# Kernel tuning notes

Measured on AMD Instinct MI355X. Metric: run time of the kernel, lower is better.

Reference implementation:

```python
import jax, jax.numpy as jnp
import numpy as np

B, N, I, D, K = 64, 16, 2048, 32, 32  # batch, num_capsule, input_num_capsule, dim_capsule, input_dim_capsule
ROUTINGS = 3
EPS = 1e-07


def squash(s):
    # squared_norm includes per-element eps before the sum, matching torch code
    sq = jnp.sum(s * s + EPS, axis=-1, keepdims=True)
    return sq * s / ((1.0 + sq) * jnp.sqrt(sq))


def setup_inputs() -> dict:
    key = jax.random.key(0)
    kx, kw = jax.random.split(key)
    x = jax.random.normal(kx, (B, I, K), dtype=jnp.float32)
    # xavier_uniform over a [N, I, D, K] tensor: fan_in = D*K (last two dims treated as matrix by torch init? torch treats dim1.. as fan) -- use gain=1 uniform bound per torch's convention: fan_in = I*D*K/... Use simple xavier over (fan_in=K, fan_out=D) receptive field I*N.
    fan_in = I * K
    fan_out = I * D  # torch: fan_in = size(1)*receptive, here just use uniform bound from full-tensor xavier
    bound = float(np.sqrt(6.0 / (fan_in + fan_out)))
    W = jax.random.uniform(kw, (N, I, D, K), minval=-bound, maxval=bound, dtype=jnp.float32)
    return {"x": x, "W": W}


def reference(x, W):
    # u_hat[b,n,i,d] = sum_k W[n,i,d,k] * x[b,i,k]
    u_hat = jnp.einsum('nidk,bik->bnid', W, x)
    b = jnp.zeros((B, N, I), dtype=u_hat.dtype)
    v = None
    for r in range(ROUTINGS):
        c = jax.nn.softmax(b, axis=1)                 # softmax over num_capsule
        s = jnp.einsum('bni,bnid->bnd', c, u_hat)     # [B, N, D]
        v = squash(s)
        if r < ROUTINGS - 1:
            a = jnp.einsum('bnid,bnd->bni', u_hat, v)
            b = b + a
    return v  # [B, N, D]
```

## Files before the change

kernel.cpp:

```cpp
#include <hip/hip_runtime.h>
#include <stdint.h>

#define Bdim 64
#define Ndim 16
#define Idim 2048
#define Ddim 32
#define Kdim 32
#define EPSV 1e-7f

#define TILE_I   4
#define TILES_PB 16
#define NB_Y     (Idim / (TILE_I * TILES_PB))

typedef __attribute__((ext_vector_type(8))) short short8v;
typedef __attribute__((ext_vector_type(4))) float f32x4;

static __device__ __forceinline__ unsigned pk_rne(float a, float b) {
    unsigned ua = __float_as_uint(a);
    unsigned ub = __float_as_uint(b);
    ua = (ua + 0x7fffu + ((ua >> 16) & 1u)) >> 16;
    ub = (ub + 0x7fffu + ((ub >> 16) & 1u)) >> 16;
    return (ua & 0xffffu) | (ub << 16);
}
static __device__ __forceinline__ float bf2f(unsigned us) {
    return __uint_as_float(us << 16);
}

#define GLL16(g, s)                                                              \
    __builtin_amdgcn_global_load_lds(                                            \
        (const __attribute__((address_space(1))) void*)(uintptr_t)(const void*)(g), \
        (__attribute__((address_space(3))) void*)(uintptr_t)(void*)(s), 16, 0, 0)

__global__ __launch_bounds__(256) void convert_x(
    const float* __restrict__ x, unsigned short* __restrict__ x2)
{
    const int i  = blockIdx.x;
    const int b  = threadIdx.x >> 2;
    const int ko = threadIdx.x & 3;
    const float* src = x + ((size_t)b * Idim + i) * Kdim + (ko << 3);
    float4 a = ((const float4*)src)[0];
    float4 c = ((const float4*)src)[1];
    uint4 o;
    o.x = pk_rne(a.x, a.y); o.y = pk_rne(a.z, a.w);
    o.z = pk_rne(c.x, c.y); o.w = pk_rne(c.z, c.w);
    *(uint4*)(x2 + ((size_t)i * 64 + b) * 32 + (ko << 3)) = o;
}

__global__ __launch_bounds__(256) void pass1_dma(
    const float* __restrict__ W, const unsigned short* __restrict__ x2,
    unsigned short* __restrict__ uhat, float* __restrict__ s0)
{
    __shared__ float          ldsW[2][TILE_I * 1024];
    __shared__ unsigned short ldsX[2][TILE_I * 2048];

    const int n     = blockIdx.x;
    const int iblk0 = blockIdx.y * (TILE_I * TILES_PB);
    const int tid   = threadIdx.x;
    const int l     = tid & 63;
    const int bcol  = ((tid >> 6) << 4) + (l & 15);
    const int krow  = l >> 4;

    const float*          Wblk = W  + ((size_t)n * Idim + iblk0) * (Ddim * Kdim);
    const unsigned short* Xblk = x2 + (size_t)iblk0 * (64 * 32);

    f32x4 acc0 = {0.f, 0.f, 0.f, 0.f};
    f32x4 acc1 = {0.f, 0.f, 0.f, 0.f};
    const f32x4 zero = {0.f, 0.f, 0.f, 0.f};

    auto stage = [&](int t, int buf) {
        const float* Wt = Wblk + (size_t)t * (TILE_I * 1024);
        float* dw = &ldsW[buf][0];
        #pragma unroll
        for (int j = 0; j < 4; ++j) {
            const int c  = j * 256 + tid;
            const int lc = c & 63, h = (c >> 6) & 1, mt = (c >> 7) & 1, il = c >> 8;
            const float* src = Wt + il * 1024 + ((mt << 4) + (lc & 15)) * 32
                                  + ((lc >> 4) << 3) + (h << 2);
            GLL16(src, dw + (size_t)c * 4);
        }
        const unsigned short* Xt = Xblk + (size_t)t * (TILE_I * 2048);
        unsigned short* dx = &ldsX[buf][0];
        #pragma unroll
        for (int j = 0; j < 4; ++j) {
            const int c = j * 256 + tid;
            GLL16(Xt + (size_t)c * 8, dx + (size_t)c * 8);
        }
    };

    stage(0, 0);

    for (int t = 0; t < TILES_PB; ++t) {
        if (t + 1 < TILES_PB) stage(t + 1, (t + 1) & 1);
        asm volatile("s_waitcnt vmcnt(8)" ::: "memory");
        __builtin_amdgcn_s_barrier();
        __builtin_amdgcn_sched_barrier(0);

        const float*          lw = &ldsW[t & 1][0];
        const unsigned short* lx = &ldsX[t & 1][0];
        const int ibase = iblk0 + t * TILE_I;

        #pragma unroll
        for (int il = 0; il < TILE_I; ++il) {
            const int i = ibase + il;

            union { short8v v; unsigned u[4]; } bf, af0, af1;
            bf.v = *(const short8v*)(lx + il * 2048 + bcol * 32 + (krow << 3));

            const float4 w00 = *(const float4*)(lw + ((il * 256 + l)       << 2));
            const float4 w01 = *(const float4*)(lw + ((il * 256 + 64 + l)  << 2));
            const float4 w10 = *(const float4*)(lw + ((il * 256 + 128 + l) << 2));
            const float4 w11 = *(const float4*)(lw + ((il * 256 + 192 + l) << 2));
            af0.u[0] = pk_rne(w00.x, w00.y); af0.u[1] = pk_rne(w00.z, w00.w);
            af0.u[2] = pk_rne(w01.x, w01.y); af0.u[3] = pk_rne(w01.z, w01.w);
            af1.u[0] = pk_rne(w10.x, w10.y); af1.u[1] = pk_rne(w10.z, w10.w);
            af1.u[2] = pk_rne(w11.x, w11.y); af1.u[3] = pk_rne(w11.z, w11.w);

            f32x4 c0 = __builtin_amdgcn_mfma_f32_16x16x32_bf16(af0.v, bf.v, zero, 0, 0, 0);
            f32x4 c1 = __builtin_amdgcn_mfma_f32_16x16x32_bf16(af1.v, bf.v, zero, 0, 0, 0);

            const size_t ubase = (((size_t)i * Ndim + n) * 64 + bcol) * Ddim + (krow << 2);
            uint2 p0; p0.x = pk_rne(c0[0], c0[1]); p0.y = pk_rne(c0[2], c0[3]);
            *(uint2*)(uhat + ubase) = p0;
            uint2 p1; p1.x = pk_rne(c1[0], c1[1]); p1.y = pk_rne(c1[2], c1[3]);
            *(uint2*)(uhat + ubase + 16) = p1;

            acc0 += c0;
            acc1 += c1;
        }
        asm volatile("s_waitcnt lgkmcnt(0)" ::: "memory");
        __builtin_amdgcn_s_barrier();
        __builtin_amdgcn_sched_barrier(0);
    }

    float* sp = s0 + ((size_t)bcol * Ndim + n) * Ddim + (krow << 2);
    #pragma unroll
    for (int r = 0; r < 4; ++r) atomicAdd(sp + r, acc0[r]);
    #pragma unroll
    for (int r = 0; r < 4; ++r) atomicAdd(sp + 16 + r, acc1[r]);
}

__global__ __launch_bounds__(256) void pass1_simple(
    const float* __restrict__ W, const float* __restrict__ x,
    unsigned short* __restrict__ uhat, float* __restrict__ s0, int bbase, int Bc)
{
    const int IB = 16;
    const int n  = blockIdx.x;
    const int i0 = blockIdx.y * IB;
    const int w  = threadIdx.x >> 6;
    const int l  = threadIdx.x & 63;
    const int bcol  = (w << 4) + (l & 15);
    const int bglob = bbase + bcol;
    const int krow  = l >> 4;

    f32x4 acc0 = {0.f,0.f,0.f,0.f}, acc1 = {0.f,0.f,0.f,0.f};
    const f32x4 zero = {0.f,0.f,0.f,0.f};

    for (int ii = 0; ii < IB; ++ii) {
        const int i = i0 + ii;
        const float* xp = x + ((size_t)bglob * Idim + i) * Kdim + (krow << 3);
        float4 xa = ((const float4*)xp)[0];
        float4 xb = ((const float4*)xp)[1];
        union { short8v v; unsigned u[4]; } bf, af0, af1;
        bf.u[0]=pk_rne(xa.x,xa.y); bf.u[1]=pk_rne(xa.z,xa.w);
        bf.u[2]=pk_rne(xb.x,xb.y); bf.u[3]=pk_rne(xb.z,xb.w);

        const float* wbase = W + ((size_t)n * Idim + i) * Ddim * Kdim + (krow << 3);
        const float* wp0 = wbase + (size_t)(l & 15) * Kdim;
        float4 wa = ((const float4*)wp0)[0];
        float4 wb = ((const float4*)wp0)[1];
        af0.u[0]=pk_rne(wa.x,wa.y); af0.u[1]=pk_rne(wa.z,wa.w);
        af0.u[2]=pk_rne(wb.x,wb.y); af0.u[3]=pk_rne(wb.z,wb.w);
        const float* wp1 = wp0 + 16 * Kdim;
        float4 wc = ((const float4*)wp1)[0];
        float4 wd = ((const float4*)wp1)[1];
        af1.u[0]=pk_rne(wc.x,wc.y); af1.u[1]=pk_rne(wc.z,wc.w);
        af1.u[2]=pk_rne(wd.x,wd.y); af1.u[3]=pk_rne(wd.z,wd.w);

        f32x4 c0 = __builtin_amdgcn_mfma_f32_16x16x32_bf16(af0.v, bf.v, zero, 0,0,0);
        f32x4 c1 = __builtin_amdgcn_mfma_f32_16x16x32_bf16(af1.v, bf.v, zero, 0,0,0);

        const size_t ubase = (((size_t)i * Ndim + n) * Bc + bcol) * Ddim + (krow << 2);
        uint2 p0; p0.x=pk_rne(c0[0],c0[1]); p0.y=pk_rne(c0[2],c0[3]);
        *(uint2*)(uhat + ubase) = p0;
        uint2 p1; p1.x=pk_rne(c1[0],c1[1]); p1.y=pk_rne(c1[2],c1[3]);
        *(uint2*)(uhat + ubase + 16) = p1;
        acc0 += c0; acc1 += c1;
    }
    float* sp = s0 + ((size_t)bglob * Ndim + n) * Ddim + (krow << 2);
    #pragma unroll
    for (int r = 0; r < 4; ++r) atomicAdd(sp + r, acc0[r]);
    #pragma unroll
    for (int r = 0; r < 4; ++r) atomicAdd(sp + 16 + r, acc1[r]);
}

template<int FIRST>
__global__ __launch_bounds__(256) void route_kernel(
    const unsigned short* __restrict__ uhat, const float* __restrict__ vin,
    float* __restrict__ bbuf, float* __restrict__ sout, int bbase, int Bc)
{
    const int bc = blockIdx.x;
    const int it = blockIdx.y;
    const int w = threadIdx.x >> 6;
    const int l = threadIdx.x & 63;
    const int g = l >> 2, q = l & 3;
    const int bglob = bbase + bc;

    const float* vp = vin + ((size_t)bglob * Ndim + g) * Ddim + (q << 3);
    float vreg[8];
    *(float4*)&vreg[0] = ((const float4*)vp)[0];
    *(float4*)&vreg[4] = ((const float4*)vp)[1];

    float sacc[8];
    #pragma unroll
    for (int j = 0; j < 8; ++j) sacc[j] = 0.f;

    for (int ii = w; ii < 128; ii += 4) {
        const int i = (it << 7) + ii;
        const unsigned short* up = uhat + (((size_t)i * Ndim + g) * Bc + bc) * Ddim + (q << 3);
        uint4 uraw = *(const uint4*)up;
        float u[8];
        u[0] = bf2f(uraw.x & 0xffffu); u[1] = bf2f(uraw.x >> 16);
        u[2] = bf2f(uraw.y & 0xffffu); u[3] = bf2f(uraw.y >> 16);
        u[4] = bf2f(uraw.z & 0xffffu); u[5] = bf2f(uraw.z >> 16);
        u[6] = bf2f(uraw.w & 0xffffu); u[7] = bf2f(uraw.w >> 16);

        float p = 0.f;
        #pragma unroll
        for (int j = 0; j < 8; ++j) p = fmaf(u[j], vreg[j], p);
        p += __shfl_xor(p, 1);
        p += __shfl_xor(p, 2);

        float logit = p;
        if (FIRST) {
            if (q == 0) bbuf[((size_t)bc * Idim + i) * Ndim + g] = p;
        } else {
            logit += bbuf[((size_t)bc * Idim + i) * Ndim + g];
        }
        float m = logit;
        m = fmaxf(m, __shfl_xor(m, 4));
        m = fmaxf(m, __shfl_xor(m, 8));
        m = fmaxf(m, __shfl_xor(m, 16));
        m = fmaxf(m, __shfl_xor(m, 32));
        float e = __expf(logit - m);
        float z = e;
        z += __shfl_xor(z, 4);
        z += __shfl_xor(z, 8);
        z += __shfl_xor(z, 16);
        z += __shfl_xor(z, 32);
        float c = e / z;

        #pragma unroll
        for (int j = 0; j < 8; ++j) sacc[j] = fmaf(c, u[j], sacc[j]);
    }

    __shared__ float sl[4][512];
    #pragma unroll
    for (int j = 0; j < 8; ++j) sl[w][(l << 3) + j] = sacc[j];
    __syncthreads();
    for (int e2 = threadIdx.x; e2 < 512; e2 += 256) {
        float vsum = sl[0][e2] + sl[1][e2] + sl[2][e2] + sl[3][e2];
        atomicAdd(sout + (size_t)bglob * (Ndim * Ddim) + e2, vsum);
    }
}

__global__ __launch_bounds__(256) void squash_kernel(
    const float* __restrict__ s, float* __restrict__ vout, float scale, int bbase)
{
    const int tid = blockIdx.x * 256 + threadIdx.x;
    const int row = tid >> 5;
    const int d   = tid & 31;
    const size_t off = ((size_t)bbase * Ndim + row) * Ddim + d;
    float sv = s[off] * scale;
    float t = fmaf(sv, sv, EPSV);
    t += __shfl_xor(t, 1);
    t += __shfl_xor(t, 2);
    t += __shfl_xor(t, 4);
    t += __shfl_xor(t, 8);
    t += __shfl_xor(t, 16);
    float vv = sv * t / ((1.f + t) * sqrtf(t));
    vout[off] = vv;
}

extern "C" void kernel_launch(void* const* d_in, const int* in_sizes, int n_in,
                              void* d_out, int out_size, void* d_ws, size_t ws_size,
                              hipStream_t stream)
{
    (void)in_sizes; (void)n_in; (void)out_size;
    const float* x = (const float*)d_in[0];
    const float* W = (const float*)d_in[1];
    float* out = (float*)d_out;

    const size_t snd = (size_t)Bdim * Ndim * Ddim;
    const size_t fixed = 5 * snd * sizeof(float);

    int Bc = 64;
    while (Bc > 16) {
        size_t need = (size_t)Bc * Idim * Ndim * Ddim * 2 + (size_t)Bc * Idim * Ndim * 4 + fixed;
        if (need <= ws_size) break;
        Bc >>= 1;
    }

    char* p = (char*)d_ws;
    unsigned short* uhat = (unsigned short*)p; p += (size_t)Bc * Idim * Ndim * Ddim * 2;
    float* bbuf = (float*)p;                   p += (size_t)Bc * Idim * Ndim * 4;
    float* sbuf = (float*)p;
    float* s0 = sbuf;
    float* s1 = sbuf + snd;
    float* s2 = sbuf + 2 * snd;
    float* v0 = sbuf + 3 * snd;
    float* v1 = sbuf + 4 * snd;

    for (int bbase = 0; bbase < Bdim; bbase += Bc) {
        (void)hipMemsetAsync(sbuf, 0, 3 * snd * sizeof(float), stream);

        if (Bc == 64) {
            unsigned short* x2 = (unsigned short*)bbuf;
            convert_x<<<dim3(Idim), 256, 0, stream>>>(x, x2);
            pass1_dma<<<dim3(Ndim, NB_Y), 256, 0, stream>>>(W, x2, uhat, s0);
        } else {
            pass1_simple<<<dim3(Ndim, Idim / 16), dim3(64 * (Bc / 16)), 0, stream>>>(
                W, x, uhat, s0, bbase, Bc);
        }
        squash_kernel<<<dim3(Bc * 2), 256, 0, stream>>>(s0, v0, 1.f / 16.f, bbase);

        route_kernel<1><<<dim3(Bc, Idim / 128), 256, 0, stream>>>(uhat, v0, bbuf, s1, bbase, Bc);
        squash_kernel<<<dim3(Bc * 2), 256, 0, stream>>>(s1, v1, 1.f, bbase);

        route_kernel<0><<<dim3(Bc, Idim / 128), 256, 0, stream>>>(uhat, v1, bbuf, s2, bbase, Bc);
        squash_kernel<<<dim3(Bc * 2), 256, 0, stream>>>(s2, out, 1.f, bbase);
    }
}
```

Measured before the change: 169.9 us.

## Deepen prefetch in GEMM tile loop and batch loads in routing loop

In the u_hat GEMM kernel, the wait on outstanding global-to-LDS loads is relaxed in middle iterations so the next tile's transfers stay in flight while the current tile is consumed. In the routing kernel, the per-i loop is restructured to issue four u_hat vector loads and four logit loads up front before computing, which raises memory-level parallelism and hides latency. This costs extra registers and, if the vmcnt accounting is wrong, could read LDS data before it has arrived.

```diff
diff --git a/kernel.cpp b/kernel.cpp
--- a/kernel.cpp
+++ b/kernel.cpp
@@ -91,7 +91,11 @@
 
     for (int t = 0; t < TILES_PB; ++t) {
         if (t + 1 < TILES_PB) stage(t + 1, (t + 1) & 1);
-        asm volatile("s_waitcnt vmcnt(8)" ::: "memory");
+        if (t == 0 || t == TILES_PB - 1) {
+            asm volatile("s_waitcnt vmcnt(8)" ::: "memory");
+        } else {
+            asm volatile("s_waitcnt vmcnt(16)" ::: "memory");
+        }
         __builtin_amdgcn_s_barrier();
         __builtin_amdgcn_sched_barrier(0);
 
@@ -214,43 +218,55 @@
     #pragma unroll
     for (int j = 0; j < 8; ++j) sacc[j] = 0.f;
 
-    for (int ii = w; ii < 128; ii += 4) {
-        const int i = (it << 7) + ii;
-        const unsigned short* up = uhat + (((size_t)i * Ndim + g) * Bc + bc) * Ddim + (q << 3);
-        uint4 uraw = *(const uint4*)up;
-        float u[8];
-        u[0] = bf2f(uraw.x & 0xffffu); u[1] = bf2f(uraw.x >> 16);
-        u[2] = bf2f(uraw.y & 0xffffu); u[3] = bf2f(uraw.y >> 16);
-        u[4] = bf2f(uraw.z & 0xffffu); u[5] = bf2f(uraw.z >> 16);
-        u[6] = bf2f(uraw.w & 0xffffu); u[7] = bf2f(uraw.w >> 16);
-
-        float p = 0.f;
-        #pragma unroll
-        for (int j = 0; j < 8; ++j) p = fmaf(u[j], vreg[j], p);
-        p += __shfl_xor(p, 1);
-        p += __shfl_xor(p, 2);
-
-        float logit = p;
-        if (FIRST) {
-            if (q == 0) bbuf[((size_t)bc * Idim + i) * Ndim + g] = p;
-        } else {
-            logit += bbuf[((size_t)bc * Idim + i) * Ndim + g];
-        }
-        float m = logit;
-        m = fmaxf(m, __shfl_xor(m, 4));
-        m = fmaxf(m, __shfl_xor(m, 8));
-        m = fmaxf(m, __shfl_xor(m, 16));
-        m = fmaxf(m, __shfl_xor(m, 32));
-        float e = __expf(logit - m);
-        float z = e;
-        z += __shfl_xor(z, 4);
-        z += __shfl_xor(z, 8);
-        z += __shfl_xor(z, 16);
-        z += __shfl_xor(z, 32);
-        float c = e / z;
-
-        #pragma unroll
-        for (int j = 0; j < 8; ++j) sacc[j] = fmaf(c, u[j], sacc[j]);
+    for (int base = 0; base < 128; base += 16) {
+        const int i0v = (it << 7) + base + w;
+
+        uint4 ur[4];
+        float bl[4];
+        #pragma unroll
+        for (int j = 0; j < 4; ++j) {
+            const int i = i0v + 4 * j;
+            ur[j] = *(const uint4*)(uhat + (((size_t)i * Ndim + g) * Bc + bc) * Ddim + (q << 3));
+            if (!FIRST) bl[j] = bbuf[((size_t)bc * Idim + i) * Ndim + g];
+        }
+
+        #pragma unroll
+        for (int j = 0; j < 4; ++j) {
+            const int i = i0v + 4 * j;
+            float u[8];
+            u[0] = bf2f(ur[j].x & 0xffffu); u[1] = bf2f(ur[j].x >> 16);
+            u[2] = bf2f(ur[j].y & 0xffffu); u[3] = bf2f(ur[j].y >> 16);
+            u[4] = bf2f(ur[j].z & 0xffffu); u[5] = bf2f(ur[j].z >> 16);
+            u[6] = bf2f(ur[j].w & 0xffffu); u[7] = bf2f(ur[j].w >> 16);
+
+            float p = 0.f;
+            #pragma unroll
+            for (int k = 0; k < 8; ++k) p = fmaf(u[k], vreg[k], p);
+            p += __shfl_xor(p, 1);
+            p += __shfl_xor(p, 2);
+
+            float logit = p;
+            if (FIRST) {
+                if (q == 0) bbuf[((size_t)bc * Idim + i) * Ndim + g] = p;
+            } else {
+                logit += bl[j];
+            }
+            float m = logit;
+            m = fmaxf(m, __shfl_xor(m, 4));
+            m = fmaxf(m, __shfl_xor(m, 8));
+            m = fmaxf(m, __shfl_xor(m, 16));
+            m = fmaxf(m, __shfl_xor(m, 32));
+            float e = __expf(logit - m);
+            float z = e;
+            z += __shfl_xor(z, 4);
+            z += __shfl_xor(z, 8);
+            z += __shfl_xor(z, 16);
+            z += __shfl_xor(z, 32);
+            float c = e / z;
+
+            #pragma unroll
+            for (int k = 0; k < 8; ++k) sacc[k] = fmaf(c, u[k], sacc[k]);
+        }
     }
 
     __shared__ float sl[4][512];
```

Result: slower. 175.6 us (+3.3%).

## Restructure pass1 to keep x tile resident and loop over capsules per block

Applied to the files above, without the earlier changes.

pass1_dma now assigns each 512-thread block a fixed block of 8 input capsules and loops over all 16 output capsules. The bf16 x tile is loaded into LDS once and reused across every n, while W tiles for successive n are double-buffered. Each wave computes one of the two 16-row D halves instead of both. The intent is to stop reloading x for every capsule and to raise per-block parallelism. In exchange the kernel launches fewer blocks, uses more LDS per block, and issues atomic adds into s0 once per capsule per block.

```diff
diff --git a/kernel.cpp b/kernel.cpp
--- a/kernel.cpp
+++ b/kernel.cpp
@@ -8,9 +8,7 @@
 #define Kdim 32
 #define EPSV 1e-7f
 
-#define TILE_I   4
-#define TILES_PB 16
-#define NB_Y     (Idim / (TILE_I * TILES_PB))
+#define IBLK8 8
 
 typedef __attribute__((ext_vector_type(8))) short short8v;
 typedef __attribute__((ext_vector_type(4))) float f32x4;
@@ -46,97 +44,93 @@
     *(uint4*)(x2 + ((size_t)i * 64 + b) * 32 + (ko << 3)) = o;
 }
 
-__global__ __launch_bounds__(256) void pass1_dma(
+__global__ __launch_bounds__(512) void pass1_dma(
     const float* __restrict__ W, const unsigned short* __restrict__ x2,
     unsigned short* __restrict__ uhat, float* __restrict__ s0)
 {
-    __shared__ float          ldsW[2][TILE_I * 1024];
-    __shared__ unsigned short ldsX[2][TILE_I * 2048];
-
-    const int n     = blockIdx.x;
-    const int iblk0 = blockIdx.y * (TILE_I * TILES_PB);
-    const int tid   = threadIdx.x;
-    const int l     = tid & 63;
-    const int bcol  = ((tid >> 6) << 4) + (l & 15);
-    const int krow  = l >> 4;
-
-    const float*          Wblk = W  + ((size_t)n * Idim + iblk0) * (Ddim * Kdim);
-    const unsigned short* Xblk = x2 + (size_t)iblk0 * (64 * 32);
-
-    f32x4 acc0 = {0.f, 0.f, 0.f, 0.f};
-    f32x4 acc1 = {0.f, 0.f, 0.f, 0.f};
+    __shared__ float          ldsW[2][IBLK8 * 1024];
+    __shared__ unsigned short ldsX[IBLK8 * 2048];
+
+    const int i0   = blockIdx.x * IBLK8;
+    const int tid  = threadIdx.x;
+    const int w    = tid >> 6;
+    const int l    = tid & 63;
+    const int brg  = w >> 1;
+    const int mt   = w & 1;
+    const int bcol = (brg << 4) + (l & 15);
+    const int krow = l >> 4;
+
     const f32x4 zero = {0.f, 0.f, 0.f, 0.f};
 
-    auto stage = [&](int t, int buf) {
-        const float* Wt = Wblk + (size_t)t * (TILE_I * 1024);
+    auto stageW = [&](int n, int buf) {
+        const float* Wt = W + ((size_t)n * Idim + i0) * 1024;
         float* dw = &ldsW[buf][0];
         #pragma unroll
         for (int j = 0; j < 4; ++j) {
-            const int c  = j * 256 + tid;
-            const int lc = c & 63, h = (c >> 6) & 1, mt = (c >> 7) & 1, il = c >> 8;
-            const float* src = Wt + il * 1024 + ((mt << 4) + (lc & 15)) * 32
-                                  + ((lc >> 4) << 3) + (h << 2);
-            GLL16(src, dw + (size_t)c * 4);
-        }
-        const unsigned short* Xt = Xblk + (size_t)t * (TILE_I * 2048);
-        unsigned short* dx = &ldsX[buf][0];
+            const int g   = w * 4 + j;
+            const int il  = g >> 2, mtc = (g >> 1) & 1, h = g & 1;
+            const float* src = Wt + il * 1024 + ((mtc << 4) + (l & 15)) * 32
+                                  + ((l >> 4) << 3) + (h << 2);
+            GLL16(src, dw + ((size_t)(g * 64 + l)) * 4);
+        }
+    };
+
+    {
+        const unsigned short* Xt = x2 + (size_t)i0 * 2048;
         #pragma unroll
         for (int j = 0; j < 4; ++j) {
-            const int c = j * 256 + tid;
-            GLL16(Xt + (size_t)c * 8, dx + (size_t)c * 8);
-        }
-    };
-
-    stage(0, 0);
-
-    for (int t = 0; t < TILES_PB; ++t) {
-        if (t + 1 < TILES_PB) stage(t + 1, (t + 1) & 1);
-        asm volatile("s_waitcnt vmcnt(8)" ::: "memory");
+            const int c = (w * 4 + j) * 64 + l;
+            GLL16(Xt + (size_t)c * 8, &ldsX[0] + (size_t)c * 8);
+        }
+        stageW(0, 0);
+        asm volatile("s_waitcnt vmcnt(0)" ::: "memory");
         __builtin_amdgcn_s_barrier();
         __builtin_amdgcn_sched_barrier(0);
-
-        const float*          lw = &ldsW[t & 1][0];
-        const unsigned short* lx = &ldsX[t & 1][0];
-        const int ibase = iblk0 + t * TILE_I;
-
-        #pragma unroll
-        for (int il = 0; il < TILE_I; ++il) {
-            const int i = ibase + il;
-
-            union { short8v v; unsigned u[4]; } bf, af0, af1;
-            bf.v = *(const short8v*)(lx + il * 2048 + bcol * 32 + (krow << 3));
-
-            const float4 w00 = *(const float4*)(lw + ((il * 256 + l)       << 2));
-            const float4 w01 = *(const float4*)(lw + ((il * 256 + 64 + l)  << 2));
-            const float4 w10 = *(const float4*)(lw + ((il * 256 + 128 + l) << 2));
-            const float4 w11 = *(const float4*)(lw + ((il * 256 + 192 + l) << 2));
-            af0.u[0] = pk_rne(w00.x, w00.y); af0.u[1] = pk_rne(w00.z, w00.w);
-            af0.u[2] = pk_rne(w01.x, w01.y); af0.u[3] = pk_rne(w01.z, w01.w);
-            af1.u[0] = pk_rne(w10.x, w10.y); af1.u[1] = pk_rne(w10.z, w10.w);
-            af1.u[2] = pk_rne(w11.x, w11.y); af1.u[3] = pk_rne(w11.z, w11.w);
-
-            f32x4 c0 = __builtin_amdgcn_mfma_f32_16x16x32_bf16(af0.v, bf.v, zero, 0, 0, 0);
-            f32x4 c1 = __builtin_amdgcn_mfma_f32_16x16x32_bf16(af1.v, bf.v, zero, 0, 0, 0);
-
-            const size_t ubase = (((size_t)i * Ndim + n) * 64 + bcol) * Ddim + (krow << 2);
-            uint2 p0; p0.x = pk_rne(c0[0], c0[1]); p0.y = pk_rne(c0[2], c0[3]);
-            *(uint2*)(uhat + ubase) = p0;
-            uint2 p1; p1.x = pk_rne(c1[0], c1[1]); p1.y = pk_rne(c1[2], c1[3]);
-            *(uint2*)(uhat + ubase + 16) = p1;
-
-            acc0 += c0;
-            acc1 += c1;
-        }
+    }
+
+    for (int n = 0; n < Ndim; ++n) {
+        if (n + 1 < Ndim) stageW(n + 1, (n + 1) & 1);
+        if (n == Ndim - 1) {
+            asm volatile("s_waitcnt vmcnt(12)" ::: "memory");
+        } else {
+            asm volatile("s_waitcnt vmcnt(16)" ::: "memory");
+        }
+        __builtin_amdgcn_s_barrier();
+        __builtin_amdgcn_sched_barrier(0);
+
+        const float* lw = &ldsW[n & 1][0];
+        f32x4 acc = {0.f, 0.f, 0.f, 0.f};
+
+        #pragma unroll
+        for (int il = 0; il < IBLK8; ++il) {
+            const int i = i0 + il;
+
+            union { short8v v; unsigned u[4]; } bf, af;
+            bf.v = *(const short8v*)(&ldsX[0] + il * 2048 + bcol * 32 + (krow << 3));
+
+            const float4 wa = *(const float4*)(lw + ((size_t)(((il << 2) + (mt << 1) + 0) * 64 + l)) * 4);
+            const float4 wb = *(const float4*)(lw + ((size_t)(((il << 2) + (mt << 1) + 1) * 64 + l)) * 4);
+            af.u[0] = pk_rne(wa.x, wa.y); af.u[1] = pk_rne(wa.z, wa.w);
+            af.u[2] = pk_rne(wb.x, wb.y); af.u[3] = pk_rne(wb.z, wb.w);
+
+            f32x4 c = __builtin_amdgcn_mfma_f32_16x16x32_bf16(af.v, bf.v, zero, 0, 0, 0);
+
+            const size_t ubase = (((size_t)i * Ndim + n) * 64 + bcol) * Ddim
+                                 + (mt << 4) + (krow << 2);
+            uint2 p; p.x = pk_rne(c[0], c[1]); p.y = pk_rne(c[2], c[3]);
+            *(uint2*)(uhat + ubase) = p;
+
+            acc += c;
+        }
+
+        float* sp = s0 + ((size_t)bcol * Ndim + n) * Ddim + (mt << 4) + (krow << 2);
+        #pragma unroll
+        for (int r = 0; r < 4; ++r) atomicAdd(sp + r, acc[r]);
+
         asm volatile("s_waitcnt lgkmcnt(0)" ::: "memory");
         __builtin_amdgcn_s_barrier();
         __builtin_amdgcn_sched_barrier(0);
     }
-
-    float* sp = s0 + ((size_t)bcol * Ndim + n) * Ddim + (krow << 2);
-    #pragma unroll
-    for (int r = 0; r < 4; ++r) atomicAdd(sp + r, acc0[r]);
-    #pragma unroll
-    for (int r = 0; r < 4; ++r) atomicAdd(sp + 16 + r, acc1[r]);
 }
 
 __global__ __launch_bounds__(256) void pass1_simple(
@@ -316,7 +310,7 @@
         if (Bc == 64) {
             unsigned short* x2 = (unsigned short*)bbuf;
             convert_x<<<dim3(Idim), 256, 0, stream>>>(x, x2);
-            pass1_dma<<<dim3(Ndim, NB_Y), 256, 0, stream>>>(W, x2, uhat, s0);
+            pass1_dma<<<dim3(Idim / IBLK8), 512, 0, stream>>>(W, x2, uhat, s0);
         } else {
             pass1_simple<<<dim3(Ndim, Idim / 16), dim3(64 * (Bc / 16)), 0, stream>>>(
                 W, x, uhat, s0, bbase, Bc);
```

New measurement: 327.3 us. 1.93x slower.

## Restructure pass1 blocks to cover four capsules and reuse staged x tiles

Applied to the files above, without the earlier changes.

The u_hat pass is retiled so that each 512-thread block handles 4 output capsules over 32 input capsules. It used to handle one capsule over 64. The bf16 x tile for each group of 4 input capsules is now staged once and reused across the 4 capsules, while W slices stream through a double buffer. Each pair of waves splits the input capsules, and their partial s0 sums are combined through LDS before the atomics, which halves the atomic traffic per block. The grid shrinks from 16x32 to 4x64 blocks. This adds more barriers per unit of work and a fine-grained vmcnt schedule that must stay correct.

```diff
diff --git a/kernel.cpp b/kernel.cpp
--- a/kernel.cpp
+++ b/kernel.cpp
@@ -7,10 +7,6 @@
 #define Ddim 32
 #define Kdim 32
 #define EPSV 1e-7f
-
-#define TILE_I   4
-#define TILES_PB 16
-#define NB_Y     (Idim / (TILE_I * TILES_PB))
 
 typedef __attribute__((ext_vector_type(8))) short short8v;
 typedef __attribute__((ext_vector_type(4))) float f32x4;
@@ -46,97 +42,133 @@
     *(uint4*)(x2 + ((size_t)i * 64 + b) * 32 + (ko << 3)) = o;
 }
 
-__global__ __launch_bounds__(256) void pass1_dma(
+__global__ __launch_bounds__(512) void pass1_dma(
     const float* __restrict__ W, const unsigned short* __restrict__ x2,
     unsigned short* __restrict__ uhat, float* __restrict__ s0)
 {
-    __shared__ float          ldsW[2][TILE_I * 1024];
-    __shared__ unsigned short ldsX[2][TILE_I * 2048];
-
-    const int n     = blockIdx.x;
-    const int iblk0 = blockIdx.y * (TILE_I * TILES_PB);
+    __shared__ float          ldsW[2][4 * 1024];
+    __shared__ unsigned short ldsX[2][4 * 2048];
+
+    const int nbase = blockIdx.x * 4;
+    const int i0    = blockIdx.y * 32;
     const int tid   = threadIdx.x;
+    const int w     = tid >> 6;
     const int l     = tid & 63;
-    const int bcol  = ((tid >> 6) << 4) + (l & 15);
+    const int brg   = w >> 1;
+    const int ih    = w & 1;
+    const int bcol  = (brg << 4) + (l & 15);
     const int krow  = l >> 4;
 
-    const float*          Wblk = W  + ((size_t)n * Idim + iblk0) * (Ddim * Kdim);
-    const unsigned short* Xblk = x2 + (size_t)iblk0 * (64 * 32);
-
-    f32x4 acc0 = {0.f, 0.f, 0.f, 0.f};
-    f32x4 acc1 = {0.f, 0.f, 0.f, 0.f};
     const f32x4 zero = {0.f, 0.f, 0.f, 0.f};
-
-    auto stage = [&](int t, int buf) {
-        const float* Wt = Wblk + (size_t)t * (TILE_I * 1024);
-        float* dw = &ldsW[buf][0];
-        #pragma unroll
-        for (int j = 0; j < 4; ++j) {
-            const int c  = j * 256 + tid;
-            const int lc = c & 63, h = (c >> 6) & 1, mt = (c >> 7) & 1, il = c >> 8;
-            const float* src = Wt + il * 1024 + ((mt << 4) + (lc & 15)) * 32
+    f32x4 acc[4][2];
+    #pragma unroll
+    for (int n = 0; n < 4; ++n) { acc[n][0] = zero; acc[n][1] = zero; }
+
+    auto stageW = [&](int uu) {
+        const int sn = uu & 3, ss = uu >> 2;
+        const float* Wq = W + (((size_t)(nbase + sn) * Idim) + i0 + ss * 4) * 1024;
+        float* dw = &ldsW[uu & 1][0];
+        #pragma unroll
+        for (int j = 0; j < 2; ++j) {
+            const int c  = j * 512 + tid;
+            const int lc = c & 63, h = (c >> 6) & 1, mtc = (c >> 7) & 1, il = c >> 8;
+            const float* src = Wq + il * 1024 + ((mtc << 4) + (lc & 15)) * 32
                                   + ((lc >> 4) << 3) + (h << 2);
             GLL16(src, dw + (size_t)c * 4);
         }
-        const unsigned short* Xt = Xblk + (size_t)t * (TILE_I * 2048);
-        unsigned short* dx = &ldsX[buf][0];
-        #pragma unroll
-        for (int j = 0; j < 4; ++j) {
-            const int c = j * 256 + tid;
-            GLL16(Xt + (size_t)c * 8, dx + (size_t)c * 8);
-        }
     };
-
-    stage(0, 0);
-
-    for (int t = 0; t < TILES_PB; ++t) {
-        if (t + 1 < TILES_PB) stage(t + 1, (t + 1) & 1);
-        asm volatile("s_waitcnt vmcnt(8)" ::: "memory");
-        __builtin_amdgcn_s_barrier();
-        __builtin_amdgcn_sched_barrier(0);
-
-        const float*          lw = &ldsW[t & 1][0];
-        const unsigned short* lx = &ldsX[t & 1][0];
-        const int ibase = iblk0 + t * TILE_I;
-
-        #pragma unroll
-        for (int il = 0; il < TILE_I; ++il) {
-            const int i = ibase + il;
-
-            union { short8v v; unsigned u[4]; } bf, af0, af1;
-            bf.v = *(const short8v*)(lx + il * 2048 + bcol * 32 + (krow << 3));
-
-            const float4 w00 = *(const float4*)(lw + ((il * 256 + l)       << 2));
-            const float4 w01 = *(const float4*)(lw + ((il * 256 + 64 + l)  << 2));
-            const float4 w10 = *(const float4*)(lw + ((il * 256 + 128 + l) << 2));
-            const float4 w11 = *(const float4*)(lw + ((il * 256 + 192 + l) << 2));
-            af0.u[0] = pk_rne(w00.x, w00.y); af0.u[1] = pk_rne(w00.z, w00.w);
-            af0.u[2] = pk_rne(w01.x, w01.y); af0.u[3] = pk_rne(w01.z, w01.w);
-            af1.u[0] = pk_rne(w10.x, w10.y); af1.u[1] = pk_rne(w10.z, w10.w);
-            af1.u[2] = pk_rne(w11.x, w11.y); af1.u[3] = pk_rne(w11.z, w11.w);
-
-            f32x4 c0 = __builtin_amdgcn_mfma_f32_16x16x32_bf16(af0.v, bf.v, zero, 0, 0, 0);
-            f32x4 c1 = __builtin_amdgcn_mfma_f32_16x16x32_bf16(af1.v, bf.v, zero, 0, 0, 0);
-
-            const size_t ubase = (((size_t)i * Ndim + n) * 64 + bcol) * Ddim + (krow << 2);
-            uint2 p0; p0.x = pk_rne(c0[0], c0[1]); p0.y = pk_rne(c0[2], c0[3]);
-            *(uint2*)(uhat + ubase) = p0;
-            uint2 p1; p1.x = pk_rne(c1[0], c1[1]); p1.y = pk_rne(c1[2], c1[3]);
-            *(uint2*)(uhat + ubase + 16) = p1;
-
-            acc0 += c0;
-            acc1 += c1;
-        }
-        asm volatile("s_waitcnt lgkmcnt(0)" ::: "memory");
-        __builtin_amdgcn_s_barrier();
-        __builtin_amdgcn_sched_barrier(0);
-    }
-
-    float* sp = s0 + ((size_t)bcol * Ndim + n) * Ddim + (krow << 2);
-    #pragma unroll
-    for (int r = 0; r < 4; ++r) atomicAdd(sp + r, acc0[r]);
-    #pragma unroll
-    for (int r = 0; r < 4; ++r) atomicAdd(sp + 16 + r, acc1[r]);
+    auto stageX = [&](int ss) {
+        const unsigned short* Xq = x2 + ((size_t)(i0 + ss * 4)) * 2048;
+        unsigned short* dx = &ldsX[ss & 1][0];
+        #pragma unroll
+        for (int j = 0; j < 2; ++j) {
+            const int c = j * 512 + tid;
+            GLL16(Xq + (size_t)c * 8, dx + (size_t)c * 8);
+        }
+    };
+
+    stageX(0); stageW(0);
+    asm volatile("s_waitcnt vmcnt(0)" ::: "memory");
+    __builtin_amdgcn_s_barrier();
+    __builtin_amdgcn_sched_barrier(0);
+
+    for (int s = 0; s < 8; ++s) {
+        #pragma unroll
+        for (int n = 0; n < 4; ++n) {
+            const int u = s * 4 + n;
+            const bool last = (u == 31);
+            if (!last) {
+                stageW(u + 1);
+                if (n == 3) stageX(s + 1);
+            }
+            if (last)        { asm volatile("s_waitcnt vmcnt(4)" ::: "memory"); }
+            else if (n == 3) { asm volatile("s_waitcnt vmcnt(8)" ::: "memory"); }
+            else             { asm volatile("s_waitcnt vmcnt(6)" ::: "memory"); }
+            __builtin_amdgcn_s_barrier();
+            __builtin_amdgcn_sched_barrier(0);
+
+            const float*          lw = &ldsW[u & 1][0];
+            const unsigned short* lx = &ldsX[s & 1][0];
+            const int ng = nbase + n;
+
+            #pragma unroll
+            for (int il2 = 0; il2 < 2; ++il2) {
+                const int il = (ih << 1) + il2;
+                const int i  = i0 + s * 4 + il;
+
+                union { short8v v; unsigned u4[4]; } bf, af0, af1;
+                bf.v = *(const short8v*)(lx + il * 2048 + bcol * 32 + (krow << 3));
+
+                const float4 w00 = *(const float4*)(lw + ((il * 256 + l)       << 2));
+                const float4 w01 = *(const float4*)(lw + ((il * 256 + 64 + l)  << 2));
+                const float4 w10 = *(const float4*)(lw + ((il * 256 + 128 + l) << 2));
+                const float4 w11 = *(const float4*)(lw + ((il * 256 + 192 + l) << 2));
+                af0.u4[0] = pk_rne(w00.x, w00.y); af0.u4[1] = pk_rne(w00.z, w00.w);
+                af0.u4[2] = pk_rne(w01.x, w01.y); af0.u4[3] = pk_rne(w01.z, w01.w);
+                af1.u4[0] = pk_rne(w10.x, w10.y); af1.u4[1] = pk_rne(w10.z, w10.w);
+                af1.u4[2] = pk_rne(w11.x, w11.y); af1.u4[3] = pk_rne(w11.z, w11.w);
+
+                f32x4 c0 = __builtin_amdgcn_mfma_f32_16x16x32_bf16(af0.v, bf.v, zero, 0, 0, 0);
+                f32x4 c1 = __builtin_amdgcn_mfma_f32_16x16x32_bf16(af1.v, bf.v, zero, 0, 0, 0);
+
+                const size_t ubase = (((size_t)i * Ndim + ng) * 64 + bcol) * Ddim + (krow << 2);
+                uint2 p0; p0.x = pk_rne(c0[0], c0[1]); p0.y = pk_rne(c0[2], c0[3]);
+                *(uint2*)(uhat + ubase) = p0;
+                uint2 p1; p1.x = pk_rne(c1[0], c1[1]); p1.y = pk_rne(c1[2], c1[3]);
+                *(uint2*)(uhat + ubase + 16) = p1;
+
+                acc[n][0] += c0;
+                acc[n][1] += c1;
+            }
+            asm volatile("s_waitcnt lgkmcnt(0)" ::: "memory");
+            __builtin_amdgcn_s_barrier();
+            __builtin_amdgcn_sched_barrier(0);
+        }
+    }
+
+    float* red = &ldsW[0][0];
+    if (ih == 1) {
+        #pragma unroll
+        for (int n = 0; n < 4; ++n) {
+            #pragma unroll
+            for (int r = 0; r < 4; ++r) {
+                red[((brg * 64 + l) * 32) + n * 8 + r]     = acc[n][0][r];
+                red[((brg * 64 + l) * 32) + n * 8 + 4 + r] = acc[n][1][r];
+            }
+        }
+    }
+    __syncthreads();
+    if (ih == 0) {
+        #pragma unroll
+        for (int n = 0; n < 4; ++n) {
+            float* sp = s0 + ((size_t)bcol * Ndim + nbase + n) * Ddim + (krow << 2);
+            #pragma unroll
+            for (int r = 0; r < 4; ++r) {
+                atomicAdd(sp + r,      acc[n][0][r] + red[((brg * 64 + l) * 32) + n * 8 + r]);
+                atomicAdd(sp + 16 + r, acc[n][1][r] + red[((brg * 64 + l) * 32) + n * 8 + 4 + r]);
+            }
+        }
+    }
 }
 
 __global__ __launch_bounds__(256) void pass1_simple(
@@ -316,7 +348,7 @@
         if (Bc == 64) {
             unsigned short* x2 = (unsigned short*)bbuf;
             convert_x<<<dim3(Idim), 256, 0, stream>>>(x, x2);
-            pass1_dma<<<dim3(Ndim, NB_Y), 256, 0, stream>>>(W, x2, uhat, s0);
+            pass1_dma<<<dim3(4, 64), 512, 0, stream>>>(W, x2, uhat, s0);
         } else {
             pass1_simple<<<dim3(Ndim, Idim / 16), dim3(64 * (Bc / 16)), 0, stream>>>(
                 W, x, uhat, s0, bbase, Bc);
```

New measurement: 179.9 us. +5.9%, slower.
